# Kernel tuning notes

Measured on AMD Instinct MI355X. Metric: run time of the kernel, lower is better.

## Reference

```python
import jax, jax.numpy as jnp
import numpy as np

EPS = 1e-6

# SIM(3) layout per lietorch: [tx,ty,tz, qx,qy,qz,qw, s]

def quat_mul(q1, q2):
    x1, y1, z1, w1 = jnp.moveaxis(q1, -1, 0)
    x2, y2, z2, w2 = jnp.moveaxis(q2, -1, 0)
    return jnp.stack([
        w1 * x2 + x1 * w2 + y1 * z2 - z1 * y2,
        w1 * y2 - x1 * z2 + y1 * w2 + z1 * x2,
        w1 * z2 + x1 * y2 - y1 * x2 + z1 * w2,
        w1 * w2 - x1 * x2 - y1 * y2 - z1 * z2,
    ], axis=-1)


def quat_rotate(q, v):
    qv, qw = q[..., :3], q[..., 3:4]
    uv = jnp.cross(qv, v)
    return v + 2.0 * (qw * uv + jnp.cross(qv, uv))


def sim3_inv(T):
    t, q, s = T[..., :3], T[..., 3:7], T[..., 7:8]
    q_inv = q * jnp.array([-1.0, -1.0, -1.0, 1.0], dtype=T.dtype)
    s_inv = 1.0 / s
    t_inv = -s_inv * quat_rotate(q_inv, t)
    return jnp.concatenate([t_inv, q_inv, s_inv], axis=-1)


def sim3_mul(T1, T2):
    t1, q1, s1 = T1[..., :3], T1[..., 3:7], T1[..., 7:8]
    t2, q2, s2 = T2[..., :3], T2[..., 3:7], T2[..., 7:8]
    t = t1 + s1 * quat_rotate(q1, t2)
    return jnp.concatenate([t, quat_mul(q1, q2), s1 * s2], axis=-1)


def skew(v):
    x, y, z = v[..., 0], v[..., 1], v[..., 2]
    O = jnp.zeros_like(x)
    return jnp.stack([
        jnp.stack([O, -z, y], -1),
        jnp.stack([z, O, -x], -1),
        jnp.stack([-y, x, O], -1),
    ], -2)


def sim3_log(T):
    t, q, s = T[..., :3], T[..., 3:7], T[..., 7:8]
    qv, qw = q[..., :3], q[..., 3:4]
    nv = jnp.linalg.norm(qv, axis=-1, keepdims=True)
    theta_r = 2.0 * jnp.arctan2(nv, qw)  # rotation angle
    small_r = nv < EPS
    fac = jnp.where(small_r, 2.0, theta_r / jnp.where(small_r, 1.0, nv))
    phi = fac * qv  # so(3) log
    sigma = jnp.log(s)

    # W = C*I + A*Phi + B*Phi^2 (Sophus/lietorch Sim3 calcW), tau = W^{-1} t
    theta = jnp.linalg.norm(phi, axis=-1, keepdims=True)
    sig_small = jnp.abs(sigma) < EPS
    th_small = theta < EPS
    sg = jnp.where(sig_small, 1.0, sigma)
    th = jnp.where(th_small, 1.0, theta)
    scale = jnp.exp(sigma)
    th2, sg2 = th * th, sg * sg
    C = jnp.where(sig_small, 1.0, (scale - 1.0) / sg)
    # sigma ~ 0 branch
    A_ss = jnp.where(th_small, 0.5, (1.0 - jnp.cos(th)) / th2)
    B_ss = jnp.where(th_small, 1.0 / 6.0, (th - jnp.sin(th)) / (th2 * th))
    # generic branch
    a = scale * jnp.sin(th)
    b = scale * jnp.cos(th)
    c = th2 + sg2
    A_g = (a * sg + (1.0 - b) * th) / (th * c)
    B_g = (C - ((b - 1.0) * sg + a * th) / c) / th2
    # theta ~ 0, sigma not small branch
    A_ts = ((sg - 1.0) * scale + 1.0) / sg2
    B_ts = (scale * (sg2 - 2.0 * sg + 2.0) - 2.0) / (2.0 * sg2 * sg)
    A = jnp.where(sig_small, A_ss, jnp.where(th_small, A_ts, A_g))
    B = jnp.where(sig_small, B_ss, jnp.where(th_small, B_ts, B_g))

    Phi = skew(phi)
    I3 = jnp.eye(3, dtype=T.dtype)
    W = C[..., None] * I3 + A[..., None] * Phi + B[..., None] * (Phi @ Phi)
    tau = jnp.linalg.solve(W, t[..., None])[..., 0]
    return jnp.concatenate([tau, phi, sigma], axis=-1)


def _rand_sim3(key, n):
    k1, k2, k3 = jax.random.split(key, 3)
    t = jax.random.normal(k1, (n, 3), dtype=jnp.float32)
    q = jax.random.normal(k2, (n, 4), dtype=jnp.float32)
    q = q / jnp.linalg.norm(q, axis=-1, keepdims=True)
    q = jnp.where(q[:, 3:4] < 0, -q, q)  # w >= 0
    s = jnp.exp(0.1 * jax.random.normal(k3, (n, 1), dtype=jnp.float32))
    return jnp.concatenate([t, q, s], axis=-1)


N_FRAME = 1_000_000
N_LC = N_FRAME - 1


def setup_inputs() -> dict:
    key = jax.random.key(0)
    ks = jax.random.split(key, 7)
    return {
        "Twc": _rand_sim3(ks[0], N_FRAME),
        "Twc_prior_inv": _rand_sim3(ks[1], N_FRAME - 1),
        "Todom_inv": _rand_sim3(ks[2], N_FRAME - 1),
        "prior_weight": jax.random.uniform(ks[3], (N_FRAME - 1, 7), dtype=jnp.float32),
        "odom_weight": jax.random.uniform(ks[4], (N_FRAME - 1, 7), dtype=jnp.float32),
        "edges": jax.random.randint(ks[5], (N_LC, 2), 0, N_FRAME),
        "T_lc": _rand_sim3(ks[6], N_LC),
    }


def reference(Twc, Twc_prior_inv, Todom_inv, prior_weight, odom_weight, edges, T_lc):
    Ti_inv = sim3_inv(Twc[:-1])
    delta = sim3_mul(Ti_inv, Twc[1:])  # Twc[:-1].Inv() * Twc[1:]
    r_prior = sim3_log(sim3_mul(delta, Twc_prior_inv)) * prior_weight
    # NOTE: source uses self.odom_Twc[1:]; in this module only self.Twc exists,
    # so odom delta uses the same pose chain.
    r_odom = sim3_log(sim3_mul(delta, Todom_inv)) * odom_weight
    residual = r_prior + r_odom
    # loop closures: gather poses by edge indices
    delta_lc = sim3_mul(sim3_inv(Twc[edges[:, 0]]), Twc[edges[:, 1]])
    r_lc = sim3_log(sim3_mul(delta_lc, T_lc))
    return residual + r_lc
```

## Files before the change

### kernel.cpp

```cpp
#include <hip/hip_runtime.h>
#include <math.h>

#define EPSF 1e-6f

typedef float v4f __attribute__((ext_vector_type(4)));
typedef int   v2i __attribute__((ext_vector_type(2)));

struct F3   { float x, y, z; };
struct Quat { float x, y, z, w; };
struct Sim3 { F3 t; Quat q; float s; };

__device__ __forceinline__ F3 cross3(F3 a, F3 b) {
    return { a.y*b.z - a.z*b.y, a.z*b.x - a.x*b.z, a.x*b.y - a.y*b.x };
}

__device__ __forceinline__ F3 quat_rotate(Quat q, F3 v) {
    F3 qv { q.x, q.y, q.z };
    F3 uv  = cross3(qv, v);
    F3 cuv = cross3(qv, uv);
    return { v.x + 2.0f*(q.w*uv.x + cuv.x),
             v.y + 2.0f*(q.w*uv.y + cuv.y),
             v.z + 2.0f*(q.w*uv.z + cuv.z) };
}

__device__ __forceinline__ Quat quat_mul(Quat a, Quat b) {
    return {
        a.w*b.x + a.x*b.w + a.y*b.z - a.z*b.y,
        a.w*b.y - a.x*b.z + a.y*b.w + a.z*b.x,
        a.w*b.z + a.x*b.y - a.y*b.x + a.z*b.w,
        a.w*b.w - a.x*b.x - a.y*b.y - a.z*b.z
    };
}

__device__ __forceinline__ Sim3 sim3_inv(Sim3 T) {
    Quat qi { -T.q.x, -T.q.y, -T.q.z, T.q.w };
    float si = __fdividef(1.0f, T.s);
    F3 r = quat_rotate(qi, T.t);
    return { { -si*r.x, -si*r.y, -si*r.z }, qi, si };
}

__device__ __forceinline__ Sim3 sim3_mul(Sim3 A, Sim3 B) {
    F3 r = quat_rotate(A.q, B.t);
    return { { A.t.x + A.s*r.x, A.t.y + A.s*r.y, A.t.z + A.s*r.z },
             quat_mul(A.q, B.q), A.s * B.s };
}

__device__ __forceinline__ Sim3 load_sim3(const float* __restrict__ p) {
    v4f a = *reinterpret_cast<const v4f*>(p);
    v4f b = *reinterpret_cast<const v4f*>(p + 4);
    return { {a.x, a.y, a.z}, {a.w, b.x, b.y, b.z}, b.w };
}

__device__ __forceinline__ Sim3 load_sim3_nt(const float* __restrict__ p) {
    v4f a = __builtin_nontemporal_load(reinterpret_cast<const v4f*>(p));
    v4f b = __builtin_nontemporal_load(reinterpret_cast<const v4f*>(p) + 1);
    return { {a.x, a.y, a.z}, {a.w, b.x, b.y, b.z}, b.w };
}

__device__ __forceinline__ float fast_atan2_pos(float y, float x) {
    float ax = fabsf(x);
    float mn = fminf(y, ax);
    float mx = fmaxf(y, ax);
    float t  = __fdividef(mn, mx);
    float s  = t * t;
    float p  = fmaf(s, 0.0208351f, -0.0851330f);
    p = fmaf(s, p,  0.1801410f);
    p = fmaf(s, p, -0.3302995f);
    p = fmaf(s, p,  0.9998660f);
    float r = t * p;
    r = (y > ax)   ? (1.5707963268f - r) : r;
    r = (x < 0.0f) ? (3.1415926536f - r) : r;
    return r;
}

__device__ __forceinline__ void sim3_log(Sim3 T, float out[7]) {
    float qx = T.q.x, qy = T.q.y, qz = T.q.z, qw = T.q.w;
    float nv = sqrtf(qx*qx + qy*qy + qz*qz);
    float theta_r = 2.0f * fast_atan2_pos(nv, qw);
    bool  nv_small = nv < EPSF;
    float fac = nv_small ? 2.0f : __fdividef(theta_r, nv);
    float px = fac*qx, py = fac*qy, pz = fac*qz;
    float sigma = __logf(T.s);
    float theta = nv_small ? 2.0f*nv : theta_r;

    bool sig_small = fabsf(sigma) < EPSF;
    bool th_small  = theta < EPSF;
    float scale = __expf(sigma);
    float A, B, C;
    if (!sig_small && !th_small) {
        float th = theta, sg = sigma;
        float th2 = th*th, sg2 = sg*sg;
        C = __fdividef(scale - 1.0f, sg);
        float sth = __sinf(th), cth = __cosf(th);
        float a = scale * sth;
        float b = scale * cth;
        float c = th2 + sg2;
        float rc = __fdividef(1.0f, c);
        A = __fdividef(fmaf(a, sg, (1.0f - b)*th), th * c);
        B = __fdividef(C - fmaf(b - 1.0f, sg, a*th) * rc, th2);
    } else {
        float sg = sig_small ? 1.0f : sigma;
        float th = th_small  ? 1.0f : theta;
        float th2 = th*th, sg2 = sg*sg;
        C = sig_small ? 1.0f : __fdividef(scale - 1.0f, sg);
        float sth = __sinf(th), cth = __cosf(th);
        float A_ss = th_small ? 0.5f : __fdividef(1.0f - cth, th2);
        float B_ss = th_small ? (1.0f/6.0f) : __fdividef(th - sth, th2 * th);
        float a = scale * sth;
        float b = scale * cth;
        float c = th2 + sg2;
        float rc = __fdividef(1.0f, c);
        float A_g = __fdividef(fmaf(a, sg, (1.0f - b)*th), th * c);
        float B_g = __fdividef(C - fmaf(b - 1.0f, sg, a*th) * rc, th2);
        float A_ts = __fdividef(fmaf(sg - 1.0f, scale, 1.0f), sg2);
        float B_ts = __fdividef(fmaf(scale, fmaf(sg, sg - 2.0f, 2.0f), -2.0f), 2.0f*sg2*sg);
        A = sig_small ? A_ss : (th_small ? A_ts : A_g);
        B = sig_small ? B_ss : (th_small ? B_ts : B_g);
    }

    float P01 = -pz, P02 =  py;
    float P10 =  pz, P12 = -px;
    float P20 = -py, P21 =  px;
    float Q00 = P01*P10 + P02*P20;
    float Q01 = P02*P21;
    float Q02 = P01*P12;
    float Q10 = P12*P20;
    float Q11 = P10*P01 + P12*P21;
    float Q12 = P10*P02;
    float Q20 = P21*P10;
    float Q21 = P20*P01;
    float Q22 = P20*P02 + P21*P12;

    float W00 = C + B*Q00,          W01 = A*P01 + B*Q01, W02 = A*P02 + B*Q02;
    float W10 = A*P10 + B*Q10,      W11 = C + B*Q11,     W12 = A*P12 + B*Q12;
    float W20 = A*P20 + B*Q20,      W21 = A*P21 + B*Q21, W22 = C + B*Q22;

    float c00 = fmaf(W11, W22, -W12*W21);
    float c01 = fmaf(W12, W20, -W10*W22);
    float c02 = fmaf(W10, W21, -W11*W20);
    float a01 = fmaf(W02, W21, -W01*W22);
    float a02 = fmaf(W01, W12, -W02*W11);
    float a11 = fmaf(W00, W22, -W02*W20);
    float a12 = fmaf(W02, W10, -W00*W12);
    float a21 = fmaf(W01, W20, -W00*W21);
    float a22 = fmaf(W00, W11, -W01*W10);
    float det = fmaf(W00, c00, fmaf(W01, c01, W02*c02));
    float idet = __fdividef(1.0f, det);
    float tx = T.t.x, ty = T.t.y, tz = T.t.z;
    out[0] = fmaf(c00, tx, fmaf(a01, ty, a02*tz)) * idet;
    out[1] = fmaf(c01, tx, fmaf(a11, ty, a12*tz)) * idet;
    out[2] = fmaf(c02, tx, fmaf(a21, ty, a22*tz)) * idet;
    out[3] = px; out[4] = py; out[5] = pz; out[6] = sigma;
}

__global__ void __launch_bounds__(256) pgo_kernel(
        const float* __restrict__ Twc,
        const float* __restrict__ Tp_inv,
        const float* __restrict__ To_inv,
        const float* __restrict__ pw,
        const float* __restrict__ ow,
        const int*   __restrict__ edges,
        const float* __restrict__ T_lc,
        float*       __restrict__ out,
        int n) {
    unsigned i = blockIdx.x * blockDim.x + threadIdx.x;
    if (i >= (unsigned)n) return;
    unsigned i8 = i * 8u;
    unsigned i7 = i * 7u;

    v2i e = __builtin_nontemporal_load(
                reinterpret_cast<const v2i*>(edges + 2u*i));
    Sim3 Ti = load_sim3(Twc + i8);
    Sim3 Tj = load_sim3(Twc + i8 + 8u);
    Sim3 Tp = load_sim3_nt(Tp_inv + i8);

    Sim3 Ta = load_sim3(Twc + (unsigned)e.x * 8u);
    Sim3 Tb = load_sim3(Twc + (unsigned)e.y * 8u);
    Sim3 To = load_sim3_nt(To_inv + i8);
    Sim3 Tl = load_sim3_nt(T_lc + i8);
    float pwv[7], owv[7];
    #pragma unroll
    for (int k = 0; k < 7; ++k)
        pwv[k] = __builtin_nontemporal_load(pw + i7 + k);
    #pragma unroll
    for (int k = 0; k < 7; ++k)
        owv[k] = __builtin_nontemporal_load(ow + i7 + k);

    Sim3 delta = sim3_mul(sim3_inv(Ti), Tj);

    float acc[7], r[7];
    sim3_log(sim3_mul(delta, Tp), r);
    #pragma unroll
    for (int k = 0; k < 7; ++k) acc[k] = r[k] * pwv[k];

    sim3_log(sim3_mul(delta, To), r);
    #pragma unroll
    for (int k = 0; k < 7; ++k) acc[k] = fmaf(r[k], owv[k], acc[k]);

    sim3_log(sim3_mul(sim3_mul(sim3_inv(Ta), Tb), Tl), r);
    #pragma unroll
    for (int k = 0; k < 7; ++k)
        out[i7 + k] = acc[k] + r[k];
}

extern "C" void kernel_launch(void* const* d_in, const int* in_sizes, int n_in,
                              void* d_out, int out_size, void* d_ws, size_t ws_size,
                              hipStream_t stream) {
    const float* Twc   = (const float*)d_in[0];
    const float* Tp    = (const float*)d_in[1];
    const float* To    = (const float*)d_in[2];
    const float* pw    = (const float*)d_in[3];
    const float* ow    = (const float*)d_in[4];
    const int*   edges = (const int*)d_in[5];
    const float* Tlc   = (const float*)d_in[6];
    float* out = (float*)d_out;

    int n = in_sizes[1] / 8;
    const int block = 256;
    int grid = (n + block - 1) / block;
    pgo_kernel<<<grid, block, 0, stream>>>(Twc, Tp, To, pw, ow, edges, Tlc, out, n);
}
```

Before: 220.9 us.

## Double-buffer streamed inputs into LDS via async global_load_lds in persistent loop

Converts the one-item-per-thread kernel into a persistent grid of 64-thread blocks. Each block walks 64-item tiles and uses global_load_lds to prefetch the next tile's prior, odometry, loop-closure and weight arrays into a double-buffered LDS region while it computes the current tile. Pose and edge loads for the next tile are also issued early, so memory latency is meant to hide behind the sim3_log arithmetic. In exchange, occupancy per CU drops sharply and the code adds full vmcnt(0) waits, a special path for the last tile, and more complex addressing.

```diff
diff --git a/kernel.cpp b/kernel.cpp
--- a/kernel.cpp
+++ b/kernel.cpp
@@ -51,9 +51,9 @@
     return { {a.x, a.y, a.z}, {a.w, b.x, b.y, b.z}, b.w };
 }
 
-__device__ __forceinline__ Sim3 load_sim3_nt(const float* __restrict__ p) {
-    v4f a = __builtin_nontemporal_load(reinterpret_cast<const v4f*>(p));
-    v4f b = __builtin_nontemporal_load(reinterpret_cast<const v4f*>(p) + 1);
+__device__ __forceinline__ Sim3 lds_sim3_split(const float* p) {
+    v4f a = *reinterpret_cast<const v4f*>(p);
+    v4f b = *reinterpret_cast<const v4f*>(p + 256);
     return { {a.x, a.y, a.z}, {a.w, b.x, b.y, b.z}, b.w };
 }
 
@@ -153,7 +153,47 @@
     out[3] = px; out[4] = py; out[5] = pz; out[6] = sigma;
 }
 
-__global__ void __launch_bounds__(256) pgo_kernel(
+#define TPo 0
+#define TOo 512
+#define TLo 1024
+#define PWo 1536
+#define OWo 2048
+#define BUF_FLOATS 2560
+
+__device__ __forceinline__ void gld16(const float* g, float* l) {
+    __builtin_amdgcn_global_load_lds(
+        (const __attribute__((address_space(1))) void*)g,
+        (__attribute__((address_space(3))) void*)l, 16, 0, 0);
+}
+
+__device__ __forceinline__ void stage_tile(
+        float* buf, unsigned tile,
+        const float* __restrict__ Tp_inv, const float* __restrict__ To_inv,
+        const float* __restrict__ T_lc,  const float* __restrict__ pw,
+        const float* __restrict__ ow, unsigned n, unsigned lane) {
+    unsigned smax = (n*8u - 4u) & ~3u;
+    unsigned b0 = tile*512u + lane*8u;
+    unsigned b1 = b0 + 4u;
+    b0 = b0 < smax ? b0 : smax;
+    b1 = b1 < smax ? b1 : smax;
+    gld16(Tp_inv + b0, buf + TPo);
+    gld16(Tp_inv + b1, buf + TPo + 256);
+    gld16(To_inv + b0, buf + TOo);
+    gld16(To_inv + b1, buf + TOo + 256);
+    gld16(T_lc  + b0, buf + TLo);
+    gld16(T_lc  + b1, buf + TLo + 256);
+    unsigned wmax = (n*7u - 4u) & ~3u;
+    unsigned w0 = tile*448u + lane*4u;
+    unsigned w1 = w0 + 256u;
+    w0 = w0 < wmax ? w0 : wmax;
+    w1 = w1 < wmax ? w1 : wmax;
+    gld16(pw + w0, buf + PWo);
+    gld16(pw + w1, buf + PWo + 256);
+    gld16(ow + w0, buf + OWo);
+    gld16(ow + w1, buf + OWo + 256);
+}
+
+__global__ void __launch_bounds__(64, 2) pgo_kernel(
         const float* __restrict__ Twc,
         const float* __restrict__ Tp_inv,
         const float* __restrict__ To_inv,
@@ -162,45 +202,90 @@
         const int*   __restrict__ edges,
         const float* __restrict__ T_lc,
         float*       __restrict__ out,
-        int n) {
-    unsigned i = blockIdx.x * blockDim.x + threadIdx.x;
-    if (i >= (unsigned)n) return;
-    unsigned i8 = i * 8u;
-    unsigned i7 = i * 7u;
-
-    v2i e = __builtin_nontemporal_load(
-                reinterpret_cast<const v2i*>(edges + 2u*i));
-    Sim3 Ti = load_sim3(Twc + i8);
-    Sim3 Tj = load_sim3(Twc + i8 + 8u);
-    Sim3 Tp = load_sim3_nt(Tp_inv + i8);
-
-    Sim3 Ta = load_sim3(Twc + (unsigned)e.x * 8u);
-    Sim3 Tb = load_sim3(Twc + (unsigned)e.y * 8u);
-    Sim3 To = load_sim3_nt(To_inv + i8);
-    Sim3 Tl = load_sim3_nt(T_lc + i8);
-    float pwv[7], owv[7];
-    #pragma unroll
-    for (int k = 0; k < 7; ++k)
-        pwv[k] = __builtin_nontemporal_load(pw + i7 + k);
-    #pragma unroll
-    for (int k = 0; k < 7; ++k)
-        owv[k] = __builtin_nontemporal_load(ow + i7 + k);
-
-    Sim3 delta = sim3_mul(sim3_inv(Ti), Tj);
-
-    float acc[7], r[7];
-    sim3_log(sim3_mul(delta, Tp), r);
-    #pragma unroll
-    for (int k = 0; k < 7; ++k) acc[k] = r[k] * pwv[k];
-
-    sim3_log(sim3_mul(delta, To), r);
-    #pragma unroll
-    for (int k = 0; k < 7; ++k) acc[k] = fmaf(r[k], owv[k], acc[k]);
-
-    sim3_log(sim3_mul(sim3_mul(sim3_inv(Ta), Tb), Tl), r);
-    #pragma unroll
-    for (int k = 0; k < 7; ++k)
-        out[i7 + k] = acc[k] + r[k];
+        int n_) {
+    __shared__ float lds[2][BUF_FLOATS];
+    const unsigned n = (unsigned)n_;
+    const unsigned lane = threadIdx.x;
+    const unsigned T = (n + 63u) >> 6;
+    const unsigned stride = gridDim.x;
+    unsigned tile = blockIdx.x;
+    if (tile >= T) return;
+
+    stage_tile(lds[0], tile, Tp_inv, To_inv, T_lc, pw, ow, n, lane);
+    unsigned it0 = tile*64u + lane;
+    unsigned ix0 = it0 < n ? it0 : (n - 1u);
+    v2i  e_cur  = *reinterpret_cast<const v2i*>(edges + 2u*ix0);
+    Sim3 Ti_cur = load_sim3(Twc + ix0*8u);
+    Sim3 Tj_cur = load_sim3(Twc + ix0*8u + 8u);
+    asm volatile("s_waitcnt vmcnt(0)" ::: "memory");
+    __builtin_amdgcn_sched_barrier(0);
+
+    unsigned cur = 0;
+    while (true) {
+        unsigned nxt = tile + stride;
+        bool hasnxt = nxt < T;
+
+        v2i e_n; Sim3 Ti_n, Tj_n;
+        if (hasnxt) {
+            stage_tile(lds[cur ^ 1u], nxt, Tp_inv, To_inv, T_lc, pw, ow, n, lane);
+            unsigned it = nxt*64u + lane;
+            unsigned ix = it < n ? it : (n - 1u);
+            e_n  = *reinterpret_cast<const v2i*>(edges + 2u*ix);
+            Ti_n = load_sim3(Twc + ix*8u);
+            Tj_n = load_sim3(Twc + ix*8u + 8u);
+        }
+        Sim3 Ta = load_sim3(Twc + (unsigned)e_cur.x * 8u);
+        Sim3 Tb = load_sim3(Twc + (unsigned)e_cur.y * 8u);
+        __builtin_amdgcn_sched_barrier(0);
+
+        unsigned item = tile*64u + lane;
+        unsigned ixc  = item < n ? item : (n - 1u);
+        Sim3 Tp_, To_, Tl_;
+        float pwv[7], owv[7];
+        if (tile == T - 1u) {
+            Tp_ = load_sim3(Tp_inv + ixc*8u);
+            To_ = load_sim3(To_inv + ixc*8u);
+            Tl_ = load_sim3(T_lc  + ixc*8u);
+            #pragma unroll
+            for (int k = 0; k < 7; ++k) {
+                pwv[k] = pw[ixc*7u + k];
+                owv[k] = ow[ixc*7u + k];
+            }
+        } else {
+            const float* B = lds[cur];
+            Tp_ = lds_sim3_split(B + TPo + lane*4u);
+            To_ = lds_sim3_split(B + TOo + lane*4u);
+            Tl_ = lds_sim3_split(B + TLo + lane*4u);
+            #pragma unroll
+            for (int k = 0; k < 7; ++k) {
+                pwv[k] = B[PWo + lane*7u + k];
+                owv[k] = B[OWo + lane*7u + k];
+            }
+        }
+
+        Sim3 delta = sim3_mul(sim3_inv(Ti_cur), Tj_cur);
+        float acc[7], r[7];
+        sim3_log(sim3_mul(delta, Tp_), r);
+        #pragma unroll
+        for (int k = 0; k < 7; ++k) acc[k] = r[k] * pwv[k];
+        sim3_log(sim3_mul(delta, To_), r);
+        #pragma unroll
+        for (int k = 0; k < 7; ++k) acc[k] = fmaf(r[k], owv[k], acc[k]);
+
+        asm volatile("s_waitcnt vmcnt(0)" ::: "memory");
+        __builtin_amdgcn_sched_barrier(0);
+
+        sim3_log(sim3_mul(sim3_mul(sim3_inv(Ta), Tb), Tl_), r);
+        if (item < n) {
+            #pragma unroll
+            for (int k = 0; k < 7; ++k)
+                out[item*7u + k] = acc[k] + r[k];
+        }
+
+        if (!hasnxt) break;
+        tile = nxt; cur ^= 1u;
+        e_cur = e_n; Ti_cur = Ti_n; Tj_cur = Tj_n;
+    }
 }
 
 extern "C" void kernel_launch(void* const* d_in, const int* in_sizes, int n_in,
@@ -216,7 +301,7 @@
     float* out = (float*)d_out;
 
     int n = in_sizes[1] / 8;
-    const int block = 256;
-    int grid = (n + block - 1) / block;
-    pgo_kernel<<<grid, block, 0, stream>>>(Twc, Tp, To, pw, ow, edges, Tlc, out, n);
-}
+    int T = (n + 63) / 64;
+    int grid = T < 2048 ? T : 2048;
+    pgo_kernel<<<grid, 64, 0, stream>>>(Twc, Tp, To, pw, ow, edges, Tlc, out, n);
+}
```

New measurement: 225.4 us. 2.0% more time.
